# Kernel tuning notes

Measured on AMD Instinct MI355X. Metric: run time of the kernel, lower is better.

## Reference

```python
import jax, jax.numpy as jnp
import numpy as np

PARENTS = [-1, 0, 0, 0, 1, 2, 3, 4, 5, 6, 7, 8, 9, 9, 9, 12, 13, 14, 16, 17, 18, 19]
NUM_JOINTS = 22
EPS = 1e-12  # matches F.normalize eps


def _cont6d_to_mat(d6):
    """6D rotation rep -> 3x3 rotation matrix (columns b1,b2,b3)."""
    a1, a2 = d6[..., :3], d6[..., 3:]
    b1 = a1 / jnp.maximum(jnp.linalg.norm(a1, axis=-1, keepdims=True), EPS)
    b2 = a2 - b1 * jnp.sum(b1 * a2, axis=-1, keepdims=True)
    b2 = b2 / jnp.maximum(jnp.linalg.norm(b2, axis=-1, keepdims=True), EPS)
    b3 = jnp.cross(b1, b2)
    return jnp.stack((b1, b2, b3), axis=-1)  # [..., 3, 3]


def setup_inputs() -> dict:
    key = jax.random.key(0)
    k1, k2, k3 = jax.random.split(key, 3)
    B, S = 32, 4096
    pred_pos = jax.random.normal(k1, (B, S, 20, 3), dtype=jnp.float32)
    gt_rot = jax.random.normal(k2, (B, S, NUM_JOINTS, 6), dtype=jnp.float32)
    offsets = jax.random.normal(k3, (NUM_JOINTS, 3), dtype=jnp.float32) * 0.2
    return {"pred_pos": pred_pos, "gt_rot": gt_rot, "offsets": offsets}


def reference(pred_pos, gt_rot, offsets):
    B, S = gt_rot.shape[:2]
    dtype = gt_rot.dtype
    rot_mats = _cont6d_to_mat(gt_rot)  # [B,S,22,3,3]
    eye = jnp.broadcast_to(jnp.eye(3, dtype=dtype), (B, S, 3, 3))

    g_rot = [None] * NUM_JOINTS
    g_pos = [None] * NUM_JOINTS
    # Root and joint 1 rotations forced to identity (canonical frame).
    g_rot[0] = eye
    g_pos[0] = jnp.zeros((B, S, 3), dtype=dtype)
    # Sequential FK chain over the fixed 22-joint tree.
    for i in range(1, NUM_JOINTS):
        p = PARENTS[i]
        local_rot = eye if i == 1 else rot_mats[:, :, i]
        g_rot[i] = jnp.einsum('bsij,bsjk->bsik', g_rot[p], local_rot)
        g_pos[i] = g_pos[p] + jnp.einsum('bsij,j->bsi', g_rot[p], offsets[i])

    gt_pos = jnp.stack(g_pos[2:NUM_JOINTS], axis=2)  # [B,S,20,3]
    dist = jnp.linalg.norm(pred_pos - gt_pos, axis=-1)  # [B,S,20]
    mpjpe_mm = dist.mean() * 1000.0
    return mpjpe_mm
```

## Files before the change

kernel.cpp:

```cpp
#include <hip/hip_runtime.h>

#define NJ 22
#define TILE 128
#define PW 121

__device__ __forceinline__ void rot6d_to_mat(float a1x, float a1y, float a1z,
                                             float a2x, float a2y, float a2z,
                                             float* R) {
    float n1 = sqrtf(a1x * a1x + a1y * a1y + a1z * a1z);
    float inv1 = 1.0f / fmaxf(n1, 1e-12f);
    float b1x = a1x * inv1, b1y = a1y * inv1, b1z = a1z * inv1;
    float d = b1x * a2x + b1y * a2y + b1z * a2z;
    float b2x = a2x - b1x * d, b2y = a2y - b1y * d, b2z = a2z - b1z * d;
    float n2 = sqrtf(b2x * b2x + b2y * b2y + b2z * b2z);
    float inv2 = 1.0f / fmaxf(n2, 1e-12f);
    b2x *= inv2; b2y *= inv2; b2z *= inv2;
    float b3x = b1y * b2z - b1z * b2y;
    float b3y = b1z * b2x - b1x * b2z;
    float b3z = b1x * b2y - b1y * b2x;
    R[0] = b1x; R[1] = b2x; R[2] = b3x;
    R[3] = b1y; R[4] = b2y; R[5] = b3y;
    R[6] = b1z; R[7] = b2z; R[8] = b3z;
}

__device__ __forceinline__ void matmul3(const float* __restrict__ A,
                                        const float* __restrict__ B,
                                        float* __restrict__ C) {
#pragma unroll
    for (int r = 0; r < 3; ++r) {
#pragma unroll
        for (int c = 0; c < 3; ++c) {
            C[r * 3 + c] = A[r * 3 + 0] * B[0 * 3 + c]
                         + A[r * 3 + 1] * B[1 * 3 + c]
                         + A[r * 3 + 2] * B[2 * 3 + c];
        }
    }
}

__global__ __launch_bounds__(128) void mpjpe_fk_kernel(
    const float4* __restrict__ pred4,
    const float4* __restrict__ rot4,
    const float* __restrict__ offsets,
    float* __restrict__ out,
    int nposes, float scale)
{
    constexpr int PAR[NJ] = {-1, 0, 0, 0, 1, 2, 3, 4, 5, 6, 7, 8, 9, 9, 9, 12, 13, 14, 16, 17, 18, 19};

    __shared__ float lds[TILE * PW];
    __shared__ float ws[2];

    const int tid  = threadIdx.x;
    const int base = blockIdx.x * TILE;
    const int pose = base + tid;

    float pf[60];
    if (pose < nposes) {
        const float4* pp = pred4 + (size_t)pose * 15;
#pragma unroll
        for (int k = 0; k < 15; ++k) {
            float4 v = pp[k];
            pf[4*k+0] = v.x; pf[4*k+1] = v.y; pf[4*k+2] = v.z; pf[4*k+3] = v.w;
        }
    }

#pragma unroll
    for (int j = 0; j < 30; ++j) {
        int n = j * TILE + tid;
        int p = n / 30;
        int q = n - p * 30;
        if (base + p < nposes) {
            float4 v = rot4[(size_t)(base + p) * 33 + 3 + q];
            float* dst = &lds[p * PW + q * 4];
            dst[0] = v.x; dst[1] = v.y; dst[2] = v.z; dst[3] = v.w;
        }
    }
    __syncthreads();

    float sum = 0.0f;
    if (pose < nposes) {
        const float* rec = &lds[tid * PW];

        float R[NJ][9];
        float P[NJ][3];

        R[0][0] = 1.f; R[0][1] = 0.f; R[0][2] = 0.f;
        R[0][3] = 0.f; R[0][4] = 1.f; R[0][5] = 0.f;
        R[0][6] = 0.f; R[0][7] = 0.f; R[0][8] = 1.f;
        P[0][0] = 0.f; P[0][1] = 0.f; P[0][2] = 0.f;

#pragma unroll
        for (int i = 1; i < NJ; ++i) {
            const int p = PAR[i];
            float ox = offsets[i * 3 + 0];
            float oy = offsets[i * 3 + 1];
            float oz = offsets[i * 3 + 2];
#pragma unroll
            for (int r = 0; r < 3; ++r) {
                P[i][r] = P[p][r] + R[p][r * 3 + 0] * ox
                                  + R[p][r * 3 + 1] * oy
                                  + R[p][r * 3 + 2] * oz;
            }
            if (i == 1) {
#pragma unroll
                for (int k = 0; k < 9; ++k) R[i][k] = R[p][k];
            } else {
                const int r0 = 6 * (i - 2);
                float M[9];
                rot6d_to_mat(rec[r0+0], rec[r0+1], rec[r0+2],
                             rec[r0+3], rec[r0+4], rec[r0+5], M);
                matmul3(R[p], M, R[i]);
            }
            if (i >= 2) {
                const int q0 = 3 * (i - 2);
                float dx = pf[q0+0] - P[i][0];
                float dy = pf[q0+1] - P[i][1];
                float dz = pf[q0+2] - P[i][2];
                sum += sqrtf(dx * dx + dy * dy + dz * dz);
            }
        }
    }

#pragma unroll
    for (int o = 32; o > 0; o >>= 1) sum += __shfl_down(sum, o, 64);

    const int lane = tid & 63;
    const int wid  = tid >> 6;
    if (lane == 0) ws[wid] = sum;
    __syncthreads();
    if (tid == 0) {
        atomicAdd(out, (ws[0] + ws[1]) * scale);
    }
}

extern "C" void kernel_launch(void* const* d_in, const int* in_sizes, int n_in,
                              void* d_out, int out_size, void* d_ws, size_t ws_size,
                              hipStream_t stream) {
    const float4* pred4 = (const float4*)d_in[0];
    const float4* rot4  = (const float4*)d_in[1];
    const float* offsets = (const float*)d_in[2];
    float* out = (float*)d_out;

    int nposes = in_sizes[1] / (NJ * 6);
    float scale = 1000.0f / ((float)nposes * 20.0f);

    hipMemsetAsync(out, 0, sizeof(float), stream);

    int grid = (nposes + TILE - 1) / TILE;
    mpjpe_fk_kernel<<<grid, 128, 0, stream>>>(pred4, rot4, offsets, out, nposes, scale);
}
```

Measured before the change: 153.2 us.

## Stage rotations and predictions through LDS in three phases with 256-thread blocks

Result: faster. 139.1 us (-9.2%).

```diff
diff --git a/kernel.cpp b/kernel.cpp
--- a/kernel.cpp
+++ b/kernel.cpp
@@ -1,8 +1,8 @@
 #include <hip/hip_runtime.h>
 
 #define NJ 22
-#define TILE 128
-#define PW 121
+#define TILE 256
+#define PW 62
 
 __device__ __forceinline__ void rot6d_to_mat(float a1x, float a1y, float a1z,
                                              float a2x, float a2y, float a2z,
@@ -37,7 +37,25 @@
     }
 }
 
-__global__ __launch_bounds__(128) void mpjpe_fk_kernel(
+__device__ __forceinline__ void stage15(const float4* __restrict__ src,
+                                        int src_stride_f4, int src_ofs_f4,
+                                        int base, int nposes, int tid,
+                                        float2* __restrict__ lds2, bool full) {
+#pragma unroll
+    for (int k = 0; k < 15; ++k) {
+        int n = k * TILE + tid;
+        int p = n / 15;
+        int q = n - p * 15;
+        if (full || base + p < nposes) {
+            float4 v = src[(size_t)(base + p) * src_stride_f4 + src_ofs_f4 + q];
+            int d = p * 31 + 2 * q;
+            lds2[d]     = make_float2(v.x, v.y);
+            lds2[d + 1] = make_float2(v.z, v.w);
+        }
+    }
+}
+
+__global__ __launch_bounds__(256, 2) void mpjpe_fk_kernel(
     const float4* __restrict__ pred4,
     const float4* __restrict__ rot4,
     const float* __restrict__ offsets,
@@ -47,49 +65,29 @@
     constexpr int PAR[NJ] = {-1, 0, 0, 0, 1, 2, 3, 4, 5, 6, 7, 8, 9, 9, 9, 12, 13, 14, 16, 17, 18, 19};
 
     __shared__ float lds[TILE * PW];
-    __shared__ float ws[2];
+    __shared__ float wsum[4];
 
     const int tid  = threadIdx.x;
     const int base = blockIdx.x * TILE;
     const int pose = base + tid;
+    const bool full   = (base + TILE) <= nposes;
+    const bool active = pose < nposes;
+    float2* lds2 = (float2*)lds;
+    const float2* myrec = (const float2*)&lds[tid * PW];
 
-    float pf[60];
-    if (pose < nposes) {
-        const float4* pp = pred4 + (size_t)pose * 15;
-#pragma unroll
-        for (int k = 0; k < 15; ++k) {
-            float4 v = pp[k];
-            pf[4*k+0] = v.x; pf[4*k+1] = v.y; pf[4*k+2] = v.z; pf[4*k+3] = v.w;
-        }
-    }
+    float R[NJ][9];
+    float P[NJ][3];
 
-#pragma unroll
-    for (int j = 0; j < 30; ++j) {
-        int n = j * TILE + tid;
-        int p = n / 30;
-        int q = n - p * 30;
-        if (base + p < nposes) {
-            float4 v = rot4[(size_t)(base + p) * 33 + 3 + q];
-            float* dst = &lds[p * PW + q * 4];
-            dst[0] = v.x; dst[1] = v.y; dst[2] = v.z; dst[3] = v.w;
-        }
-    }
+    stage15(rot4, 33, 3, base, nposes, tid, lds2, full);
     __syncthreads();
 
-    float sum = 0.0f;
-    if (pose < nposes) {
-        const float* rec = &lds[tid * PW];
-
-        float R[NJ][9];
-        float P[NJ][3];
-
+    if (active) {
         R[0][0] = 1.f; R[0][1] = 0.f; R[0][2] = 0.f;
         R[0][3] = 0.f; R[0][4] = 1.f; R[0][5] = 0.f;
         R[0][6] = 0.f; R[0][7] = 0.f; R[0][8] = 1.f;
         P[0][0] = 0.f; P[0][1] = 0.f; P[0][2] = 0.f;
-
 #pragma unroll
-        for (int i = 1; i < NJ; ++i) {
+        for (int i = 1; i <= 11; ++i) {
             const int p = PAR[i];
             float ox = offsets[i * 3 + 0];
             float oy = offsets[i * 3 + 1];
@@ -104,19 +102,66 @@
 #pragma unroll
                 for (int k = 0; k < 9; ++k) R[i][k] = R[p][k];
             } else {
-                const int r0 = 6 * (i - 2);
+                const int s = 3 * (i - 2);
+                float2 v0 = myrec[s + 0];
+                float2 v1 = myrec[s + 1];
+                float2 v2 = myrec[s + 2];
                 float M[9];
-                rot6d_to_mat(rec[r0+0], rec[r0+1], rec[r0+2],
-                             rec[r0+3], rec[r0+4], rec[r0+5], M);
+                rot6d_to_mat(v0.x, v0.y, v1.x, v1.y, v2.x, v2.y, M);
                 matmul3(R[p], M, R[i]);
             }
-            if (i >= 2) {
-                const int q0 = 3 * (i - 2);
-                float dx = pf[q0+0] - P[i][0];
-                float dy = pf[q0+1] - P[i][1];
-                float dz = pf[q0+2] - P[i][2];
-                sum += sqrtf(dx * dx + dy * dy + dz * dz);
+        }
+    }
+    __syncthreads();
+
+    stage15(rot4, 33, 18, base, nposes, tid, lds2, full);
+    __syncthreads();
+
+    if (active) {
+#pragma unroll
+        for (int i = 12; i < NJ; ++i) {
+            const int p = PAR[i];
+            float ox = offsets[i * 3 + 0];
+            float oy = offsets[i * 3 + 1];
+            float oz = offsets[i * 3 + 2];
+#pragma unroll
+            for (int r = 0; r < 3; ++r) {
+                P[i][r] = P[p][r] + R[p][r * 3 + 0] * ox
+                                  + R[p][r * 3 + 1] * oy
+                                  + R[p][r * 3 + 2] * oz;
             }
+            if (i < NJ - 1) {
+                const int s = 3 * (i - 12);
+                float2 v0 = myrec[s + 0];
+                float2 v1 = myrec[s + 1];
+                float2 v2 = myrec[s + 2];
+                float M[9];
+                rot6d_to_mat(v0.x, v0.y, v1.x, v1.y, v2.x, v2.y, M);
+                matmul3(R[p], M, R[i]);
+            }
+        }
+    }
+    __syncthreads();
+
+    stage15(pred4, 15, 0, base, nposes, tid, lds2, full);
+    __syncthreads();
+
+    float sum = 0.0f;
+    if (active) {
+        float pf[60];
+#pragma unroll
+        for (int k = 0; k < 30; ++k) {
+            float2 v = myrec[k];
+            pf[2 * k]     = v.x;
+            pf[2 * k + 1] = v.y;
+        }
+#pragma unroll
+        for (int j = 2; j < NJ; ++j) {
+            const int f = 3 * (j - 2);
+            float dx = pf[f + 0] - P[j][0];
+            float dy = pf[f + 1] - P[j][1];
+            float dz = pf[f + 2] - P[j][2];
+            sum += sqrtf(dx * dx + dy * dy + dz * dz);
         }
     }
 
@@ -125,10 +170,10 @@
 
     const int lane = tid & 63;
     const int wid  = tid >> 6;
-    if (lane == 0) ws[wid] = sum;
+    if (lane == 0) wsum[wid] = sum;
     __syncthreads();
     if (tid == 0) {
-        atomicAdd(out, (ws[0] + ws[1]) * scale);
+        atomicAdd(out, (wsum[0] + wsum[1] + wsum[2] + wsum[3]) * scale);
     }
 }
 
@@ -146,5 +191,5 @@
     hipMemsetAsync(out, 0, sizeof(float), stream);
 
     int grid = (nposes + TILE - 1) / TILE;
-    mpjpe_fk_kernel<<<grid, 128, 0, stream>>>(pred4, rot4, offsets, out, nposes, scale);
+    mpjpe_fk_kernel<<<grid, 256, 0, stream>>>(pred4, rot4, offsets, out, nposes, scale);
 }
```

## Stage rotation tiles via direct global-to-LDS loads with wider blocks

Applied to the files above, without the earlier changes.

Result: faster. 136.2 us (-11.1%).

```diff
diff --git a/kernel.cpp b/kernel.cpp
--- a/kernel.cpp
+++ b/kernel.cpp
@@ -1,8 +1,10 @@
 #include <hip/hip_runtime.h>
 
 #define NJ 22
-#define TILE 128
-#define PW 121
+#define TILE 112
+#define RECB 528
+#define STAGE_BYTES (TILE * RECB)
+#define NCHUNK (STAGE_BYTES / 256)
 
 __device__ __forceinline__ void rot6d_to_mat(float a1x, float a1y, float a1z,
                                              float a2x, float a2y, float a2z,
@@ -37,24 +39,79 @@
     }
 }
 
-__global__ __launch_bounds__(128) void mpjpe_fk_kernel(
+__device__ __forceinline__ void g2lds4(const void* g, void* l) {
+    __builtin_amdgcn_global_load_lds(
+        (const __attribute__((address_space(1))) unsigned int*)g,
+        (__attribute__((address_space(3))) unsigned int*)l,
+        4, 0, 0);
+}
+
+__device__ __forceinline__ float fk_dist_sum(const float2* __restrict__ rec,
+                                             const float* __restrict__ pf,
+                                             const float* __restrict__ off) {
+    constexpr int PAR[NJ] = {-1, 0, 0, 0, 1, 2, 3, 4, 5, 6, 7, 8, 9, 9, 9, 12, 13, 14, 16, 17, 18, 19};
+    float R[NJ][9];
+    float P[NJ][3];
+    R[0][0] = 1.f; R[0][1] = 0.f; R[0][2] = 0.f;
+    R[0][3] = 0.f; R[0][4] = 1.f; R[0][5] = 0.f;
+    R[0][6] = 0.f; R[0][7] = 0.f; R[0][8] = 1.f;
+    P[0][0] = 0.f; P[0][1] = 0.f; P[0][2] = 0.f;
+
+    float sum = 0.0f;
+#pragma unroll
+    for (int i = 1; i < NJ; ++i) {
+        const int p = PAR[i];
+        float ox = off[i * 3 + 0];
+        float oy = off[i * 3 + 1];
+        float oz = off[i * 3 + 2];
+#pragma unroll
+        for (int r = 0; r < 3; ++r) {
+            P[i][r] = P[p][r] + R[p][r * 3 + 0] * ox
+                              + R[p][r * 3 + 1] * oy
+                              + R[p][r * 3 + 2] * oz;
+        }
+        if (i == 1) {
+#pragma unroll
+            for (int k = 0; k < 9; ++k) R[i][k] = R[p][k];
+        } else if (i < NJ - 1) {
+            const int s = 3 * (i - 2);
+            float2 v0 = rec[s + 0];
+            float2 v1 = rec[s + 1];
+            float2 v2 = rec[s + 2];
+            float M[9];
+            rot6d_to_mat(v0.x, v0.y, v1.x, v1.y, v2.x, v2.y, M);
+            matmul3(R[p], M, R[i]);
+        }
+        if (i >= 2) {
+            const int f = 3 * (i - 2);
+            float dx = pf[f + 0] - P[i][0];
+            float dy = pf[f + 1] - P[i][1];
+            float dz = pf[f + 2] - P[i][2];
+            sum += sqrtf(dx * dx + dy * dy + dz * dz);
+        }
+    }
+    return sum;
+}
+
+__global__ __launch_bounds__(256) void mpjpe_fk_kernel(
     const float4* __restrict__ pred4,
-    const float4* __restrict__ rot4,
+    const float* __restrict__ gt_rot,
     const float* __restrict__ offsets,
     float* __restrict__ out,
     int nposes, float scale)
 {
-    constexpr int PAR[NJ] = {-1, 0, 0, 0, 1, 2, 3, 4, 5, 6, 7, 8, 9, 9, 9, 12, 13, 14, 16, 17, 18, 19};
-
-    __shared__ float lds[TILE * PW];
-    __shared__ float ws[2];
+    __shared__ char smem[STAGE_BYTES];
+    __shared__ float wsum[4];
 
     const int tid  = threadIdx.x;
+    const int lane = tid & 63;
+    const int wid  = tid >> 6;
     const int base = blockIdx.x * TILE;
     const int pose = base + tid;
+    const bool mine = (tid < TILE) && (pose < nposes);
 
     float pf[60];
-    if (pose < nposes) {
+    if (mine) {
         const float4* pp = pred4 + (size_t)pose * 15;
 #pragma unroll
         for (int k = 0; k < 15; ++k) {
@@ -62,81 +119,46 @@
             pf[4*k+0] = v.x; pf[4*k+1] = v.y; pf[4*k+2] = v.z; pf[4*k+3] = v.w;
         }
     }
-
-#pragma unroll
-    for (int j = 0; j < 30; ++j) {
-        int n = j * TILE + tid;
-        int p = n / 30;
-        int q = n - p * 30;
-        if (base + p < nposes) {
-            float4 v = rot4[(size_t)(base + p) * 33 + 3 + q];
-            float* dst = &lds[p * PW + q * 4];
-            dst[0] = v.x; dst[1] = v.y; dst[2] = v.z; dst[3] = v.w;
-        }
-    }
-    __syncthreads();
+    __builtin_amdgcn_sched_barrier(0);
 
     float sum = 0.0f;
-    if (pose < nposes) {
-        const float* rec = &lds[tid * PW];
 
-        float R[NJ][9];
-        float P[NJ][3];
+    if (base + TILE <= nposes) {
+        const char* gbase = (const char*)gt_rot + (size_t)base * RECB;
+        for (int n = wid; n < NCHUNK; n += 4) {
+            g2lds4(gbase + n * 256 + lane * 4, smem + n * 256);
+        }
+        __syncthreads();
 
-        R[0][0] = 1.f; R[0][1] = 0.f; R[0][2] = 0.f;
-        R[0][3] = 0.f; R[0][4] = 1.f; R[0][5] = 0.f;
-        R[0][6] = 0.f; R[0][7] = 0.f; R[0][8] = 1.f;
-        P[0][0] = 0.f; P[0][1] = 0.f; P[0][2] = 0.f;
-
+        if (tid < TILE) {
+            const float2* rec = (const float2*)(smem + tid * RECB + 48);
+            sum = fk_dist_sum(rec, pf, offsets);
+        }
+    } else {
+        if (mine) {
+            const float2* g2 = (const float2*)(gt_rot + (size_t)pose * 132 + 12);
+            float2 lr[30];
 #pragma unroll
-        for (int i = 1; i < NJ; ++i) {
-            const int p = PAR[i];
-            float ox = offsets[i * 3 + 0];
-            float oy = offsets[i * 3 + 1];
-            float oz = offsets[i * 3 + 2];
-#pragma unroll
-            for (int r = 0; r < 3; ++r) {
-                P[i][r] = P[p][r] + R[p][r * 3 + 0] * ox
-                                  + R[p][r * 3 + 1] * oy
-                                  + R[p][r * 3 + 2] * oz;
-            }
-            if (i == 1) {
-#pragma unroll
-                for (int k = 0; k < 9; ++k) R[i][k] = R[p][k];
-            } else {
-                const int r0 = 6 * (i - 2);
-                float M[9];
-                rot6d_to_mat(rec[r0+0], rec[r0+1], rec[r0+2],
-                             rec[r0+3], rec[r0+4], rec[r0+5], M);
-                matmul3(R[p], M, R[i]);
-            }
-            if (i >= 2) {
-                const int q0 = 3 * (i - 2);
-                float dx = pf[q0+0] - P[i][0];
-                float dy = pf[q0+1] - P[i][1];
-                float dz = pf[q0+2] - P[i][2];
-                sum += sqrtf(dx * dx + dy * dy + dz * dz);
-            }
+            for (int k = 0; k < 30; ++k) lr[k] = g2[k];
+            sum = fk_dist_sum(lr, pf, offsets);
         }
     }
 
 #pragma unroll
     for (int o = 32; o > 0; o >>= 1) sum += __shfl_down(sum, o, 64);
 
-    const int lane = tid & 63;
-    const int wid  = tid >> 6;
-    if (lane == 0) ws[wid] = sum;
+    if (lane == 0) wsum[wid] = sum;
     __syncthreads();
     if (tid == 0) {
-        atomicAdd(out, (ws[0] + ws[1]) * scale);
+        atomicAdd(out, (wsum[0] + wsum[1] + wsum[2] + wsum[3]) * scale);
     }
 }
 
 extern "C" void kernel_launch(void* const* d_in, const int* in_sizes, int n_in,
                               void* d_out, int out_size, void* d_ws, size_t ws_size,
                               hipStream_t stream) {
-    const float4* pred4 = (const float4*)d_in[0];
-    const float4* rot4  = (const float4*)d_in[1];
+    const float4* pred4  = (const float4*)d_in[0];
+    const float* gt_rot  = (const float*)d_in[1];
     const float* offsets = (const float*)d_in[2];
     float* out = (float*)d_out;
 
@@ -146,5 +168,5 @@
     hipMemsetAsync(out, 0, sizeof(float), stream);
 
     int grid = (nposes + TILE - 1) / TILE;
-    mpjpe_fk_kernel<<<grid, 128, 0, stream>>>(pred4, rot4, offsets, out, nposes, scale);
+    mpjpe_fk_kernel<<<grid, 256, 0, stream>>>(pred4, gt_rot, offsets, out, nposes, scale);
 }
```
